# Kernel optimization log

Measured on AMD Instinct MI355X. Metric: run time of the kernel, lower is better.

Reference implementation:

```python
import jax, jax.numpy as jnp
import numpy as np

N_NODES = 100000
N_EDGES = 1600000
IN_CH, HID_CH, OUT_CH = 128, 64, 32


def setup_inputs() -> dict:
    key = jax.random.key(0)
    k1, k2, k3, k4 = jax.random.split(key, 4)
    x = jax.random.normal(k1, (N_NODES, IN_CH), dtype=jnp.float32)
    edge_index = jax.random.randint(k2, (2, N_EDGES), 0, N_NODES, dtype=jnp.int32)
    # Glorot-ish scaling like PyG's GCNConv init
    W1 = jax.random.normal(k3, (IN_CH, HID_CH), dtype=jnp.float32) / np.sqrt(IN_CH)
    b1 = jnp.zeros((HID_CH,), dtype=jnp.float32)
    W2 = jax.random.normal(k4, (HID_CH, OUT_CH), dtype=jnp.float32) / np.sqrt(HID_CH)
    b2 = jnp.zeros((OUT_CH,), dtype=jnp.float32)
    return {"x": x, "edge_index": edge_index, "W1": W1, "b1": b1, "W2": W2, "b2": b2}


def reference(x, edge_index, W1, b1, W2, b2):
    # PyG GCNConv semantics: add self-loops, symmetric deg^{-1/2} normalization,
    # linear transform, scatter-add aggregation to destination nodes, add bias.
    N = x.shape[0]
    loops = jnp.arange(N, dtype=edge_index.dtype)
    src = jnp.concatenate([edge_index[0], loops])  # [E+N]
    dst = jnp.concatenate([edge_index[1], loops])  # [E+N]

    deg = jax.ops.segment_sum(jnp.ones_like(src, dtype=x.dtype), dst, num_segments=N)
    dis = jnp.where(deg > 0, jax.lax.rsqrt(jnp.maximum(deg, 1.0)), 0.0)  # deg^{-1/2}
    norm = (dis[src] * dis[dst])[:, None]  # [E+N, 1]

    def gcn_conv(h, W, b):
        h = h @ W                                   # [N, C_out]
        msgs = h[src] * norm                        # gather + scale, [E+N, C_out]
        return jax.ops.segment_sum(msgs, dst, num_segments=N) + b

    h = jax.nn.relu(gcn_conv(x, W1, b1))
    # dropout is identity in eval mode (training=False)
    return gcn_conv(h, W2, b2)
```

## Files before the change

### kernel.cpp

```cpp
#include <hip/hip_runtime.h>
#include <hip/hip_bf16.h>

#define IN_CH 128
#define HID_CH 64
#define OUT_CH 32
#define EPB 2048
#define MAXB 512

typedef unsigned short ushort_t;
typedef __attribute__((ext_vector_type(8))) short short8;
typedef __attribute__((ext_vector_type(4))) float float4v;

static __device__ __forceinline__ ushort_t f2bf(float f) {
    unsigned u = __float_as_uint(f);
    unsigned r = (u + 0x7fff + ((u >> 16) & 1)) >> 16;
    return (ushort_t)r;
}
static __device__ __forceinline__ float bf_lo(unsigned u) { return __uint_as_float(u << 16); }
static __device__ __forceinline__ float bf_hi(unsigned u) { return __uint_as_float(u & 0xffff0000u); }


__global__ __launch_bounds__(256) void k_partition(const int* __restrict__ src,
                                                   const int* __restrict__ dst,
                                                   int* __restrict__ gcursor,
                                                   unsigned* __restrict__ pairs,
                                                   int E, int nbk, int cap) {
    __shared__ int lhist[MAXB];
    __shared__ int lbase[MAXB];
    __shared__ int lcur[MAXB];
    const int tid = threadIdx.x;
    for (int b = tid; b < nbk; b += 256) { lhist[b] = 0; lcur[b] = 0; }
    __syncthreads();
    int s[8], d[8];
    const int e0 = blockIdx.x * EPB;
#pragma unroll
    for (int j = 0; j < 8; ++j) {
        int e = e0 + j * 256 + tid;
        if (e < E) {
            s[j] = src[e];
            d[j] = dst[e];
            atomicAdd(&lhist[d[j] >> 8], 1);
        } else {
            d[j] = -1;
        }
    }
    __syncthreads();
    for (int b = tid; b < nbk; b += 256)
        lbase[b] = lhist[b] ? atomicAdd(&gcursor[b], lhist[b]) : 0;
    __syncthreads();
#pragma unroll
    for (int j = 0; j < 8; ++j) {
        if (d[j] >= 0) {
            int b = d[j] >> 8;
            int loc = atomicAdd(&lcur[b], 1);
            int idx = lbase[b] + loc;
            if (idx < cap)
                pairs[(long long)b * cap + idx] = ((unsigned)s[j] << 8) | (unsigned)(d[j] & 255);
        }
    }
}

__global__ __launch_bounds__(512) void k_bscan(const int* __restrict__ gcursor,
                                               int* __restrict__ bbase,
                                               int* __restrict__ rowptr,
                                               int nbk, int cap, int N) {
    __shared__ int s[512];
    const int tid = threadIdx.x;
    int v = (tid < nbk) ? min(gcursor[tid], cap) : 0;
    s[tid] = v;
    __syncthreads();
    for (int off = 1; off < 512; off <<= 1) {
        int val = (tid >= off) ? s[tid - off] : 0;
        __syncthreads();
        s[tid] += val;
        __syncthreads();
    }
    if (tid < nbk) bbase[tid] = s[tid] - v;
    if (tid == nbk - 1) rowptr[N] = s[tid];
}

__global__ __launch_bounds__(256) void k_bucket_build(const unsigned* __restrict__ pairs,
                                                      const int* __restrict__ gcursor,
                                                      const int* __restrict__ bbase,
                                                      int* __restrict__ rowptr,
                                                      int* __restrict__ col,
                                                      float* __restrict__ dis,
                                                      int cap, int N) {
    __shared__ int lc[256];
    __shared__ int ls[256];
    __shared__ int lcur[256];
    const int b = blockIdx.x, tid = threadIdx.x;
    lc[tid] = 0;
    __syncthreads();
    const int cnt = min(gcursor[b], cap);
    const int base = bbase[b];
    const unsigned* p = pairs + (long long)b * cap;
    for (int i = tid; i < cnt; i += 256) atomicAdd(&lc[p[i] & 255], 1);
    __syncthreads();
    const int v = lc[tid];
    ls[tid] = v;
    __syncthreads();
    for (int off = 1; off < 256; off <<= 1) {
        int val = (tid >= off) ? ls[tid - off] : 0;
        __syncthreads();
        ls[tid] += val;
        __syncthreads();
    }
    const int excl = ls[tid] - v;
    const int row = b * 256 + tid;
    if (row < N) {
        rowptr[row] = base + excl;
        dis[row] = rsqrtf((float)(v + 1));
    }
    lcur[tid] = base + excl;
    __syncthreads();
    for (int i = tid; i < cnt; i += 256) {
        unsigned pk = p[i];
        int pos = atomicAdd(&lcur[pk & 255], 1);
        col[pos] = (int)(pk >> 8);
    }
}


__global__ __launch_bounds__(256) void k_prepW(const float* __restrict__ W,
                                               unsigned* __restrict__ wsW,
                                               int* __restrict__ gcursor) {
    int s = blockIdx.x * 256 + threadIdx.x;
    if (s < MAXB) gcursor[s] = 0;
    if (s >= 1024) return;
    int lane = s & 63;
    int nt = (s >> 6) & 3;
    int kc = s >> 8;
    int c = nt * 16 + (lane & 15);
    int k0 = kc * 32 + (lane >> 4) * 8;
    unsigned o[4];
#pragma unroll
    for (int d = 0; d < 4; ++d) {
        unsigned lo = f2bf(W[(k0 + 2 * d) * 64 + c]);
        unsigned hi = f2bf(W[(k0 + 2 * d + 1) * 64 + c]);
        o[d] = lo | (hi << 16);
    }
    ((uint4*)wsW)[s] = make_uint4(o[0], o[1], o[2], o[3]);
}


__global__ __launch_bounds__(256) void k_mm1(const float* __restrict__ X,
                                             const unsigned* __restrict__ wsW,
                                             ushort_t* __restrict__ H, int N) {
    const int tid = threadIdx.x;
    const int wv = tid >> 6, lane = tid & 63;
    const int quad = lane >> 4, n16 = lane & 15;
    const int rowbase = blockIdx.x * 64 + wv * 16;
    const int myrow = rowbase + n16;
    const bool rok = (myrow < N);

    float4v acc0 = {}, acc1 = {}, acc2 = {}, acc3 = {};

#pragma unroll
    for (int kc = 0; kc < 4; ++kc) {
        float4 xa = make_float4(0.f, 0.f, 0.f, 0.f), xb = xa;
        if (rok) {
            const float4* p = (const float4*)(X + (long long)myrow * 128 + kc * 32 + quad * 8);
            xa = p[0];
            xb = p[1];
        }
        unsigned pk[4];
        pk[0] = (unsigned)f2bf(xa.x) | ((unsigned)f2bf(xa.y) << 16);
        pk[1] = (unsigned)f2bf(xa.z) | ((unsigned)f2bf(xa.w) << 16);
        pk[2] = (unsigned)f2bf(xb.x) | ((unsigned)f2bf(xb.y) << 16);
        pk[3] = (unsigned)f2bf(xb.z) | ((unsigned)f2bf(xb.w) << 16);
        short8 a;
        a[0] = (short)(pk[0] & 0xffff); a[1] = (short)(pk[0] >> 16);
        a[2] = (short)(pk[1] & 0xffff); a[3] = (short)(pk[1] >> 16);
        a[4] = (short)(pk[2] & 0xffff); a[5] = (short)(pk[2] >> 16);
        a[6] = (short)(pk[3] & 0xffff); a[7] = (short)(pk[3] >> 16);

        const short8* wb = (const short8*)wsW;
        short8 b0 = wb[(kc * 4 + 0) * 64 + lane];
        short8 b1 = wb[(kc * 4 + 1) * 64 + lane];
        short8 b2 = wb[(kc * 4 + 2) * 64 + lane];
        short8 b3 = wb[(kc * 4 + 3) * 64 + lane];

        acc0 = __builtin_amdgcn_mfma_f32_16x16x32_bf16(a, b0, acc0, 0, 0, 0);
        acc1 = __builtin_amdgcn_mfma_f32_16x16x32_bf16(a, b1, acc1, 0, 0, 0);
        acc2 = __builtin_amdgcn_mfma_f32_16x16x32_bf16(a, b2, acc2, 0, 0, 0);
        acc3 = __builtin_amdgcn_mfma_f32_16x16x32_bf16(a, b3, acc3, 0, 0, 0);
    }

#pragma unroll
    for (int i = 0; i < 4; ++i) {
        int row = rowbase + quad * 4 + i;
        if (row < N) {
            long long o = (long long)row * 64 + n16;
            H[o]      = f2bf(acc0[i]);
            H[o + 16] = f2bf(acc1[i]);
            H[o + 32] = f2bf(acc2[i]);
            H[o + 48] = f2bf(acc3[i]);
        }
    }
}


__global__ __launch_bounds__(256) void k_agg64_mm2(const unsigned* __restrict__ h,
                                                   const int* __restrict__ rowptr,
                                                   const int* __restrict__ col,
                                                   const float* __restrict__ dis,
                                                   const float* __restrict__ b1,
                                                   const float* __restrict__ W2,
                                                   unsigned* __restrict__ h2, int N) {
    __shared__ float zbuf[4][64];
    const int wv = threadIdx.x >> 6, lane = threadIdx.x & 63;
    const int t = lane & 31, g = lane >> 5;

    float w[32];
#pragma unroll
    for (int k = 0; k < 32; ++k) w[k] = W2[(g * 32 + k) * 32 + t];
    const float2 bv = ((const float2*)b1)[t];

    const int wave0 = blockIdx.x * 4 + wv;
    const int nwaves = gridDim.x * 4;

    for (int row = wave0; row < N; row += nwaves) {
        const int start = rowptr[row];
        const int deg = rowptr[row + 1] - start;
        const float dr = dis[row];

        int myCol = row;
        float myDis = 0.f;
        if (lane < deg) {
            myCol = col[start + lane];
            myDis = dis[myCol];
        }

        unsigned us = h[row * 32 + t];
        float w0s = g ? 0.f : dr;
        float ax = w0s * bf_lo(us), ay = w0s * bf_hi(us);

        const int cnt = min(deg, 64);
        for (int k0 = 0; k0 < cnt; k0 += 16) {
#pragma unroll
            for (int u = 0; u < 8; ++u) {
                int slot = k0 + 2 * u + g;
                int s = __shfl(myCol, slot);
                float ww = __shfl(myDis, slot);
                unsigned uu = h[s * 32 + t];
                ax += ww * bf_lo(uu);
                ay += ww * bf_hi(uu);
            }
        }
        for (int j = start + 64 + g; j < start + deg; j += 2) {
            int s = col[j];
            float ww = dis[s];
            unsigned uu = h[s * 32 + t];
            ax += ww * bf_lo(uu);
            ay += ww * bf_hi(uu);
        }
        ax += __shfl_down(ax, 32);
        ay += __shfl_down(ay, 32);

        if (!g) {
            float2 zv;
            zv.x = bv.x + dr * ax;
            zv.y = bv.y + dr * ay;
            *(float2*)&zbuf[wv][2 * t] = zv;
        }
        __builtin_amdgcn_wave_barrier();

        float acc = 0.f;
        const float* zp = &zbuf[wv][g * 32];
#pragma unroll
        for (int k = 0; k < 32; k += 4) {
            float4 zv = *(const float4*)(zp + k);
            acc += fmaxf(zv.x, 0.f) * w[k] + fmaxf(zv.y, 0.f) * w[k + 1] +
                   fmaxf(zv.z, 0.f) * w[k + 2] + fmaxf(zv.w, 0.f) * w[k + 3];
        }
        __builtin_amdgcn_wave_barrier();
        acc += __shfl_down(acc, 32);

        float o0 = __shfl(acc, 2 * t);
        float o1 = __shfl(acc, 2 * t + 1);
        if (lane < 16)
            h2[row * 16 + lane] = (unsigned)f2bf(o0) | ((unsigned)f2bf(o1) << 16);
    }
}


__global__ __launch_bounds__(256) void k_agg32(const unsigned* __restrict__ h,
                                               const int* __restrict__ rowptr,
                                               const int* __restrict__ col,
                                               const float* __restrict__ dis,
                                               const float* __restrict__ b,
                                               float* __restrict__ out, int N) {
    const int wave = (blockIdx.x * 256 + threadIdx.x) >> 6;
    const int lane = threadIdx.x & 63;
    if (wave >= N) return;
    const int row = wave;
    const int t = lane & 15, g = lane >> 4;
    const int start = rowptr[row];
    const int deg = rowptr[row + 1] - start;
    const float dr = dis[row];

    int myCol = row;
    float myDis = 0.f;
    if (lane < deg) {
        myCol = col[start + lane];
        myDis = dis[myCol];
    }

    unsigned us = h[row * 16 + t];
    float w0s = (g == 0) ? dr : 0.f;
    float ax = w0s * bf_lo(us), ay = w0s * bf_hi(us);

    const int cnt = min(deg, 64);
    for (int k0 = 0; k0 < cnt; k0 += 32) {
#pragma unroll
        for (int u = 0; u < 8; ++u) {
            int slot = k0 + 4 * u + g;
            int s = __shfl(myCol, slot);
            float w = __shfl(myDis, slot);
            unsigned uu = h[s * 16 + t];
            ax += w * bf_lo(uu);
            ay += w * bf_hi(uu);
        }
    }
    for (int j = start + 64 + g; j < start + deg; j += 4) {
        int s = col[j];
        float w = dis[s];
        unsigned uu = h[s * 16 + t];
        ax += w * bf_lo(uu);
        ay += w * bf_hi(uu);
    }
    ax += __shfl_down(ax, 32);
    ay += __shfl_down(ay, 32);
    ax += __shfl_down(ax, 16);
    ay += __shfl_down(ay, 16);
    if (!g) {
        float2 bv = ((const float2*)b)[t];
        float2 o;
        o.x = bv.x + dr * ax;
        o.y = bv.y + dr * ay;
        ((float2*)out)[row * 16 + t] = o;
    }
}

extern "C" void kernel_launch(void* const* d_in, const int* in_sizes, int n_in,
                              void* d_out, int out_size, void* d_ws, size_t ws_size,
                              hipStream_t stream) {
    const float* x  = (const float*)d_in[0];
    const int*   ei = (const int*)d_in[1];
    const float* W1 = (const float*)d_in[2];
    const float* b1 = (const float*)d_in[3];
    const float* W2 = (const float*)d_in[4];
    const float* b2 = (const float*)d_in[5];
    float* out = (float*)d_out;

    const int N = in_sizes[0] / IN_CH;
    const int E = in_sizes[1] / 2;
    const int* esrc = ei;
    const int* edst = ei + E;

    int nbk = (N + 255) >> 8;
    if (nbk > MAXB) nbk = MAXB;
    const int per_b = (E + nbk - 1) / nbk;
    const int cap = per_b + per_b / 4 + 256;

    int* rowptr   = (int*)d_ws;
    int* gcursor  = rowptr + (((N + 1) + 15) & ~15);
    int* bbase    = gcursor + MAXB;
    unsigned* wsW = (unsigned*)(bbase + MAXB);
    int* col      = (int*)(wsW + 4096);
    float* dis    = (float*)(col + ((E + 15) & ~15));
    ushort_t* h1  = (ushort_t*)(dis + ((N + 15) & ~15));
    unsigned* scratch = (unsigned*)(h1 + (((long long)N * 64 + 31) & ~31LL));
    unsigned* pairs = scratch;
    unsigned* h2    = scratch;

    const int B = 256;

    k_prepW<<<4, B, 0, stream>>>(W1, wsW, gcursor);
    k_partition<<<(E + EPB - 1) / EPB, B, 0, stream>>>(esrc, edst, gcursor, pairs, E, nbk, cap);
    k_bscan<<<1, 512, 0, stream>>>(gcursor, bbase, rowptr, nbk, cap, N);
    k_bucket_build<<<nbk, B, 0, stream>>>(pairs, gcursor, bbase, rowptr, col, dis, cap, N);

    k_mm1<<<(N + 63) / 64, B, 0, stream>>>(x, wsW, h1, N);

    const int fblocks = (N + 31) / 32;
    k_agg64_mm2<<<fblocks, B, 0, stream>>>((const unsigned*)h1, rowptr, col, dis, b1, W2, h2, N);

    k_agg32<<<((long long)N * 64 + B - 1) / B, B, 0, stream>>>((const unsigned*)h2, rowptr, col, dis, b2, out, N);
}
```

Before: 251.8 us.

## Fuse prep kernels into partition/bucket build and widen aggregation loads

W1 bf16 packing moves into extra blocks of the partition kernel, and the cursor zeroing becomes a memset. The bucket-base scan kernel is removed: each bucket-build block now redoes the 512-entry scan itself. Both aggregation kernels now load uint2 (four bf16 values) per lane and handle more neighbours at once, using an extra shuffle-reduction stage. The layer-2 weights are staged in shared memory instead of 32 registers per thread. Together these cut launches and per-gather instructions, at the cost of duplicated scan work in every bucket block.

```diff
diff --git a/kernel.cpp b/kernel.cpp
--- a/kernel.cpp
+++ b/kernel.cpp
@@ -24,11 +24,32 @@
                                                    const int* __restrict__ dst,
                                                    int* __restrict__ gcursor,
                                                    unsigned* __restrict__ pairs,
-                                                   int E, int nbk, int cap) {
+                                                   int E, int nbk, int cap, int PB,
+                                                   const float* __restrict__ W1,
+                                                   unsigned* __restrict__ wsW) {
     __shared__ int lhist[MAXB];
     __shared__ int lbase[MAXB];
     __shared__ int lcur[MAXB];
     const int tid = threadIdx.x;
+
+    if (blockIdx.x >= PB) {
+        int s = (blockIdx.x - PB) * 256 + tid;
+        int lane = s & 63;
+        int nt = (s >> 6) & 3;
+        int kc = s >> 8;
+        int c = nt * 16 + (lane & 15);
+        int k0 = kc * 32 + (lane >> 4) * 8;
+        unsigned o[4];
+#pragma unroll
+        for (int d = 0; d < 4; ++d) {
+            unsigned lo = f2bf(W1[(k0 + 2 * d) * 64 + c]);
+            unsigned hi = f2bf(W1[(k0 + 2 * d + 1) * 64 + c]);
+            o[d] = lo | (hi << 16);
+        }
+        ((uint4*)wsW)[s] = make_uint4(o[0], o[1], o[2], o[3]);
+        return;
+    }
+
     for (int b = tid; b < nbk; b += 256) { lhist[b] = 0; lcur[b] = 0; }
     __syncthreads();
     int s[8], d[8];
@@ -60,28 +81,9 @@
     }
 }
 
-__global__ __launch_bounds__(512) void k_bscan(const int* __restrict__ gcursor,
-                                               int* __restrict__ bbase,
-                                               int* __restrict__ rowptr,
-                                               int nbk, int cap, int N) {
-    __shared__ int s[512];
-    const int tid = threadIdx.x;
-    int v = (tid < nbk) ? min(gcursor[tid], cap) : 0;
-    s[tid] = v;
-    __syncthreads();
-    for (int off = 1; off < 512; off <<= 1) {
-        int val = (tid >= off) ? s[tid - off] : 0;
-        __syncthreads();
-        s[tid] += val;
-        __syncthreads();
-    }
-    if (tid < nbk) bbase[tid] = s[tid] - v;
-    if (tid == nbk - 1) rowptr[N] = s[tid];
-}
 
 __global__ __launch_bounds__(256) void k_bucket_build(const unsigned* __restrict__ pairs,
                                                       const int* __restrict__ gcursor,
-                                                      const int* __restrict__ bbase,
                                                       int* __restrict__ rowptr,
                                                       int* __restrict__ col,
                                                       float* __restrict__ dis,
@@ -90,15 +92,10 @@
     __shared__ int ls[256];
     __shared__ int lcur[256];
     const int b = blockIdx.x, tid = threadIdx.x;
-    lc[tid] = 0;
-    __syncthreads();
-    const int cnt = min(gcursor[b], cap);
-    const int base = bbase[b];
-    const unsigned* p = pairs + (long long)b * cap;
-    for (int i = tid; i < cnt; i += 256) atomicAdd(&lc[p[i] & 255], 1);
-    __syncthreads();
-    const int v = lc[tid];
-    ls[tid] = v;
+
+    int ga = min(gcursor[2 * tid], cap);
+    int gb = min(gcursor[2 * tid + 1], cap);
+    ls[tid] = ga + gb;
     __syncthreads();
     for (int off = 1; off < 256; off <<= 1) {
         int val = (tid >= off) ? ls[tid - off] : 0;
@@ -106,6 +103,27 @@
         ls[tid] += val;
         __syncthreads();
     }
+    const int p = b >> 1;
+    const int base = (p ? ls[p - 1] : 0) + ((b & 1) ? min(gcursor[b - 1], cap) : 0);
+    const int total = ls[255];
+    __syncthreads();
+    if (b == 0 && tid == 0) rowptr[N] = total;
+
+    lc[tid] = 0;
+    __syncthreads();
+    const int cnt = min(gcursor[b], cap);
+    const unsigned* pp = pairs + (long long)b * cap;
+    for (int i = tid; i < cnt; i += 256) atomicAdd(&lc[pp[i] & 255], 1);
+    __syncthreads();
+    const int v = lc[tid];
+    ls[tid] = v;
+    __syncthreads();
+    for (int off = 1; off < 256; off <<= 1) {
+        int val = (tid >= off) ? ls[tid - off] : 0;
+        __syncthreads();
+        ls[tid] += val;
+        __syncthreads();
+    }
     const int excl = ls[tid] - v;
     const int row = b * 256 + tid;
     if (row < N) {
@@ -115,32 +133,10 @@
     lcur[tid] = base + excl;
     __syncthreads();
     for (int i = tid; i < cnt; i += 256) {
-        unsigned pk = p[i];
+        unsigned pk = pp[i];
         int pos = atomicAdd(&lcur[pk & 255], 1);
         col[pos] = (int)(pk >> 8);
     }
-}
-
-
-__global__ __launch_bounds__(256) void k_prepW(const float* __restrict__ W,
-                                               unsigned* __restrict__ wsW,
-                                               int* __restrict__ gcursor) {
-    int s = blockIdx.x * 256 + threadIdx.x;
-    if (s < MAXB) gcursor[s] = 0;
-    if (s >= 1024) return;
-    int lane = s & 63;
-    int nt = (s >> 6) & 3;
-    int kc = s >> 8;
-    int c = nt * 16 + (lane & 15);
-    int k0 = kc * 32 + (lane >> 4) * 8;
-    unsigned o[4];
-#pragma unroll
-    for (int d = 0; d < 4; ++d) {
-        unsigned lo = f2bf(W[(k0 + 2 * d) * 64 + c]);
-        unsigned hi = f2bf(W[(k0 + 2 * d + 1) * 64 + c]);
-        o[d] = lo | (hi << 16);
-    }
-    ((uint4*)wsW)[s] = make_uint4(o[0], o[1], o[2], o[3]);
 }
 
 
@@ -209,16 +205,19 @@
                                                    const float* __restrict__ W2,
                                                    unsigned* __restrict__ h2, int N) {
     __shared__ float zbuf[4][64];
-    const int wv = threadIdx.x >> 6, lane = threadIdx.x & 63;
-    const int t = lane & 31, g = lane >> 5;
-
-    float w[32];
-#pragma unroll
-    for (int k = 0; k < 32; ++k) w[k] = W2[(g * 32 + k) * 32 + t];
-    const float2 bv = ((const float2*)b1)[t];
+    __shared__ float sW2[64 * 32];
+    const int tid = threadIdx.x;
+    for (int i = tid; i < 512; i += 256) ((float4*)sW2)[i] = ((const float4*)W2)[i];
+    __syncthreads();
+
+    const int wv = tid >> 6, lane = tid & 63;
+    const int t = lane & 15, g = lane >> 4;
+    const int c32 = lane & 31, kh = lane >> 5;
+    const float4 bq = ((const float4*)b1)[t];
 
     const int wave0 = blockIdx.x * 4 + wv;
     const int nwaves = gridDim.x * 4;
+    const uint2* h2w = (const uint2*)h;
 
     for (int row = wave0; row < N; row += nwaves) {
         const int start = rowptr[row];
@@ -232,55 +231,62 @@
             myDis = dis[myCol];
         }
 
-        unsigned us = h[row * 32 + t];
-        float w0s = g ? 0.f : dr;
-        float ax = w0s * bf_lo(us), ay = w0s * bf_hi(us);
+        uint2 us = h2w[row * 16 + t];
+        float w0 = (g == 0) ? dr : 0.f;
+        float a0 = w0 * bf_lo(us.x), a1 = w0 * bf_hi(us.x);
+        float a2 = w0 * bf_lo(us.y), a3 = w0 * bf_hi(us.y);
 
         const int cnt = min(deg, 64);
         for (int k0 = 0; k0 < cnt; k0 += 16) {
 #pragma unroll
-            for (int u = 0; u < 8; ++u) {
-                int slot = k0 + 2 * u + g;
+            for (int u = 0; u < 4; ++u) {
+                int slot = k0 + 4 * u + g;
                 int s = __shfl(myCol, slot);
-                float ww = __shfl(myDis, slot);
-                unsigned uu = h[s * 32 + t];
-                ax += ww * bf_lo(uu);
-                ay += ww * bf_hi(uu);
+                float f = __shfl(myDis, slot);
+                uint2 uu = h2w[s * 16 + t];
+                a0 += f * bf_lo(uu.x); a1 += f * bf_hi(uu.x);
+                a2 += f * bf_lo(uu.y); a3 += f * bf_hi(uu.y);
             }
         }
-        for (int j = start + 64 + g; j < start + deg; j += 2) {
+        for (int j = start + 64 + g; j < start + deg; j += 4) {
             int s = col[j];
-            float ww = dis[s];
-            unsigned uu = h[s * 32 + t];
-            ax += ww * bf_lo(uu);
-            ay += ww * bf_hi(uu);
-        }
-        ax += __shfl_down(ax, 32);
-        ay += __shfl_down(ay, 32);
-
-        if (!g) {
-            float2 zv;
-            zv.x = bv.x + dr * ax;
-            zv.y = bv.y + dr * ay;
-            *(float2*)&zbuf[wv][2 * t] = zv;
+            float f = dis[s];
+            uint2 uu = h2w[s * 16 + t];
+            a0 += f * bf_lo(uu.x); a1 += f * bf_hi(uu.x);
+            a2 += f * bf_lo(uu.y); a3 += f * bf_hi(uu.y);
+        }
+        a0 += __shfl_down(a0, 32); a1 += __shfl_down(a1, 32);
+        a2 += __shfl_down(a2, 32); a3 += __shfl_down(a3, 32);
+        a0 += __shfl_down(a0, 16); a1 += __shfl_down(a1, 16);
+        a2 += __shfl_down(a2, 16); a3 += __shfl_down(a3, 16);
+
+        if (lane < 16) {
+            float4 zq;
+            zq.x = bq.x + dr * a0;
+            zq.y = bq.y + dr * a1;
+            zq.z = bq.z + dr * a2;
+            zq.w = bq.w + dr * a3;
+            *(float4*)&zbuf[wv][4 * t] = zq;
         }
         __builtin_amdgcn_wave_barrier();
 
         float acc = 0.f;
-        const float* zp = &zbuf[wv][g * 32];
+        const float* zp = &zbuf[wv][kh * 32];
+        const float* wp = &sW2[kh * 32 * 32 + c32];
 #pragma unroll
         for (int k = 0; k < 32; k += 4) {
             float4 zv = *(const float4*)(zp + k);
-            acc += fmaxf(zv.x, 0.f) * w[k] + fmaxf(zv.y, 0.f) * w[k + 1] +
-                   fmaxf(zv.z, 0.f) * w[k + 2] + fmaxf(zv.w, 0.f) * w[k + 3];
+            acc += fmaxf(zv.x, 0.f) * wp[k * 32] + fmaxf(zv.y, 0.f) * wp[(k + 1) * 32] +
+                   fmaxf(zv.z, 0.f) * wp[(k + 2) * 32] + fmaxf(zv.w, 0.f) * wp[(k + 3) * 32];
         }
         __builtin_amdgcn_wave_barrier();
         acc += __shfl_down(acc, 32);
 
-        float o0 = __shfl(acc, 2 * t);
-        float o1 = __shfl(acc, 2 * t + 1);
+        const int tt = lane & 15;
+        float o0 = __shfl(acc, 2 * tt);
+        float o1 = __shfl(acc, 2 * tt + 1);
         if (lane < 16)
-            h2[row * 16 + lane] = (unsigned)f2bf(o0) | ((unsigned)f2bf(o1) << 16);
+            h2[row * 16 + tt] = (unsigned)f2bf(o0) | ((unsigned)f2bf(o1) << 16);
     }
 }
 
@@ -295,7 +301,8 @@
     const int lane = threadIdx.x & 63;
     if (wave >= N) return;
     const int row = wave;
-    const int t = lane & 15, g = lane >> 4;
+    const int t = lane & 7, g = lane >> 3;
+
     const int start = rowptr[row];
     const int deg = rowptr[row + 1] - start;
     const float dr = dis[row];
@@ -307,39 +314,46 @@
         myDis = dis[myCol];
     }
 
-    unsigned us = h[row * 16 + t];
-    float w0s = (g == 0) ? dr : 0.f;
-    float ax = w0s * bf_lo(us), ay = w0s * bf_hi(us);
+    const uint2* hw = (const uint2*)h;
+    uint2 us = hw[row * 8 + t];
+    float w0 = (g == 0) ? dr : 0.f;
+    float a0 = w0 * bf_lo(us.x), a1 = w0 * bf_hi(us.x);
+    float a2 = w0 * bf_lo(us.y), a3 = w0 * bf_hi(us.y);
 
     const int cnt = min(deg, 64);
     for (int k0 = 0; k0 < cnt; k0 += 32) {
 #pragma unroll
-        for (int u = 0; u < 8; ++u) {
-            int slot = k0 + 4 * u + g;
+        for (int u = 0; u < 4; ++u) {
+            int slot = k0 + 8 * u + g;
             int s = __shfl(myCol, slot);
-            float w = __shfl(myDis, slot);
-            unsigned uu = h[s * 16 + t];
-            ax += w * bf_lo(uu);
-            ay += w * bf_hi(uu);
-        }
-    }
-    for (int j = start + 64 + g; j < start + deg; j += 4) {
+            float f = __shfl(myDis, slot);
+            uint2 uu = hw[s * 8 + t];
+            a0 += f * bf_lo(uu.x); a1 += f * bf_hi(uu.x);
+            a2 += f * bf_lo(uu.y); a3 += f * bf_hi(uu.y);
+        }
+    }
+    for (int j = start + 64 + g; j < start + deg; j += 8) {
         int s = col[j];
-        float w = dis[s];
-        unsigned uu = h[s * 16 + t];
-        ax += w * bf_lo(uu);
-        ay += w * bf_hi(uu);
-    }
-    ax += __shfl_down(ax, 32);
-    ay += __shfl_down(ay, 32);
-    ax += __shfl_down(ax, 16);
-    ay += __shfl_down(ay, 16);
-    if (!g) {
-        float2 bv = ((const float2*)b)[t];
-        float2 o;
-        o.x = bv.x + dr * ax;
-        o.y = bv.y + dr * ay;
-        ((float2*)out)[row * 16 + t] = o;
+        float f = dis[s];
+        uint2 uu = hw[s * 8 + t];
+        a0 += f * bf_lo(uu.x); a1 += f * bf_hi(uu.x);
+        a2 += f * bf_lo(uu.y); a3 += f * bf_hi(uu.y);
+    }
+    a0 += __shfl_down(a0, 32); a1 += __shfl_down(a1, 32);
+    a2 += __shfl_down(a2, 32); a3 += __shfl_down(a3, 32);
+    a0 += __shfl_down(a0, 16); a1 += __shfl_down(a1, 16);
+    a2 += __shfl_down(a2, 16); a3 += __shfl_down(a3, 16);
+    a0 += __shfl_down(a0, 8);  a1 += __shfl_down(a1, 8);
+    a2 += __shfl_down(a2, 8);  a3 += __shfl_down(a3, 8);
+
+    if (lane < 8) {
+        float4 bq = ((const float4*)b)[t];
+        float4 o;
+        o.x = bq.x + dr * a0;
+        o.y = bq.y + dr * a1;
+        o.z = bq.z + dr * a2;
+        o.w = bq.w + dr * a3;
+        ((float4*)out)[(long long)row * 8 + t] = o;
     }
 }
 
@@ -366,8 +380,7 @@
 
     int* rowptr   = (int*)d_ws;
     int* gcursor  = rowptr + (((N + 1) + 15) & ~15);
-    int* bbase    = gcursor + MAXB;
-    unsigned* wsW = (unsigned*)(bbase + MAXB);
+    unsigned* wsW = (unsigned*)(gcursor + MAXB);
     int* col      = (int*)(wsW + 4096);
     float* dis    = (float*)(col + ((E + 15) & ~15));
     ushort_t* h1  = (ushort_t*)(dis + ((N + 15) & ~15));
@@ -376,16 +389,16 @@
     unsigned* h2    = scratch;
 
     const int B = 256;
-
-    k_prepW<<<4, B, 0, stream>>>(W1, wsW, gcursor);
-    k_partition<<<(E + EPB - 1) / EPB, B, 0, stream>>>(esrc, edst, gcursor, pairs, E, nbk, cap);
-    k_bscan<<<1, 512, 0, stream>>>(gcursor, bbase, rowptr, nbk, cap, N);
-    k_bucket_build<<<nbk, B, 0, stream>>>(pairs, gcursor, bbase, rowptr, col, dis, cap, N);
+    const int PB = (E + EPB - 1) / EPB;
+
+    hipMemsetAsync(gcursor, 0, MAXB * sizeof(int), stream);
+    k_partition<<<PB + 4, B, 0, stream>>>(esrc, edst, gcursor, pairs, E, nbk, cap, PB, W1, wsW);
+    k_bucket_build<<<nbk, B, 0, stream>>>(pairs, gcursor, rowptr, col, dis, cap, N);
 
     k_mm1<<<(N + 63) / 64, B, 0, stream>>>(x, wsW, h1, N);
 
     const int fblocks = (N + 31) / 32;
     k_agg64_mm2<<<fblocks, B, 0, stream>>>((const unsigned*)h1, rowptr, col, dis, b1, W2, h2, N);
 
-    k_agg32<<<((long long)N * 64 + B - 1) / B, B, 0, stream>>>((const unsigned*)h2, rowptr, col, dis, b2, out, N);
-}
+    k_agg32<<<(int)(((long long)N * 64 + B - 1) / B), B, 0, stream>>>((const unsigned*)h2, rowptr, col, dis, b2, out, N);
+}
```

New measurement: 249.2 us. No clear change (-1.0%).
